# Performance work log

Measured on AMD Instinct MI355X. Metric: run time of the kernel, lower is better.

Reference implementation:

```python
import jax, jax.numpy as jnp
import numpy as np

B, NPG, DEG = 512, 128, 16          # graphs, nodes/graph, out-degree
N = B * NPG                          # 65536 nodes
E = N * DEG                          # 1048576 edges
IN_DIM, HID, HEADS = 11, 32, 4
K1 = int(np.ceil(0.8 * NPG))         # 103 nodes/graph after pool1
K2 = int(np.ceil(0.8 * K1))          # 83 nodes/graph after pool2


def gat_conv(x, src, dst, mask, W, a_s, a_d, b, n_nodes):
    # PyG GATConv (concat=True, add_self_loops=True, eval mode -> no dropout)
    xp = (x @ W).reshape(n_nodes, HEADS, HID)            # [N,H,C]
    as_ = jnp.einsum('nhc,hc->nh', xp, a_s)
    ad_ = jnp.einsum('nhc,hc->nh', xp, a_d)
    loop = jnp.arange(n_nodes)
    s = jnp.concatenate([src, loop])
    d = jnp.concatenate([dst, loop])
    m = jnp.concatenate([mask, jnp.ones(n_nodes, bool)])
    logit = jax.nn.leaky_relu(as_[s] + ad_[d], 0.2)      # [E+N,H]
    logit = jnp.where(m[:, None], logit, -1e9)
    mx = jax.ops.segment_max(logit, d, num_segments=n_nodes)
    ex = jnp.exp(logit - mx[d]) * m[:, None]
    den = jax.ops.segment_sum(ex, d, num_segments=n_nodes)
    alpha = ex / (den[d] + 1e-16)                        # segment softmax over dst
    out = jax.ops.segment_sum(alpha[:, :, None] * xp[s], d, num_segments=n_nodes)
    return out.reshape(n_nodes, HEADS * HID) + b


def topk_pool(x, src, dst, mask, w, npg, k):
    # PyG TopKPooling: score = tanh((x*w).sum(-1)/||w||); keep top ceil(ratio*n) per graph
    nb = x.shape[0] // npg
    score = jnp.tanh((x @ w) / jnp.linalg.norm(w))
    vals, idx = jax.lax.top_k(score.reshape(nb, npg), k)  # [B,k]
    perm = (idx + (jnp.arange(nb) * npg)[:, None]).reshape(-1)
    x_new = x[perm] * vals.reshape(-1, 1)
    remap = jnp.full(nb * npg, -1).at[perm].set(jnp.arange(nb * k))
    ns, nd = remap[src], remap[dst]
    m = mask & (ns >= 0) & (nd >= 0)
    return x_new, jnp.where(m, ns, 0), jnp.where(m, nd, 0), m


def setup_inputs():
    key = jax.random.key(0)
    ks = jax.random.split(key, 24)
    s = 0.05
    x = jax.random.normal(ks[0], (N, IN_DIM), jnp.float32)
    src = jnp.repeat(jnp.arange(N), DEG)
    dst = (src // NPG) * NPG + jax.random.randint(ks[1], (E,), 0, NPG)
    edge_index = jnp.stack([src, dst])
    edge_attr = jax.random.normal(ks[2], (E, 4), jnp.float32)
    batch = jnp.repeat(jnp.arange(B), NPG)
    p = dict(
        W_g1=jax.random.normal(ks[3], (IN_DIM, HEADS * HID), jnp.float32) * s,
        att_src1=jax.random.normal(ks[4], (HEADS, HID), jnp.float32) * s,
        att_dst1=jax.random.normal(ks[5], (HEADS, HID), jnp.float32) * s,
        b_g1=jnp.zeros((HEADS * HID,), jnp.float32),
        W_t1=jax.random.normal(ks[6], (HEADS * HID, HID), jnp.float32) * s,
        b_t1=jnp.zeros((HID,), jnp.float32),
        pool_w1=jax.random.normal(ks[7], (HID,), jnp.float32) * s,
        W_g2=jax.random.normal(ks[8], (HID, HEADS * HID), jnp.float32) * s,
        att_src2=jax.random.normal(ks[9], (HEADS, HID), jnp.float32) * s,
        att_dst2=jax.random.normal(ks[10], (HEADS, HID), jnp.float32) * s,
        b_g2=jnp.zeros((HEADS * HID,), jnp.float32),
        W_t2=jax.random.normal(ks[11], (HEADS * HID, HID), jnp.float32) * s,
        b_t2=jnp.zeros((HID,), jnp.float32),
        pool_w2=jax.random.normal(ks[12], (HID,), jnp.float32) * s,
        W_l1=jax.random.normal(ks[13], (2 * HID, 256), jnp.float32) * s,
        b_l1=jnp.zeros((256,), jnp.float32),
        W_l2=jax.random.normal(ks[14], (256, 1024), jnp.float32) * s,
        b_l2=jnp.zeros((1024,), jnp.float32),
        W_l3=jax.random.normal(ks[15], (1024, 1), jnp.float32) * s,
        b_l3=jnp.zeros((1,), jnp.float32),
    )
    return dict(x=x, edge_index=edge_index, edge_attr=edge_attr, batch=batch, **p)


def reference(x, edge_index, edge_attr, batch,
              W_g1, att_src1, att_dst1, b_g1, W_t1, b_t1, pool_w1,
              W_g2, att_src2, att_dst2, b_g2, W_t2, b_t2, pool_w2,
              W_l1, b_l1, W_l2, b_l2, W_l3, b_l3):
    # edge_attr is ignored (GATConv built without edge_dim); batch is implicit
    # in the fixed equal-size graph layout.  Eval mode -> dropout disabled.
    src, dst = edge_index[0], edge_index[1]
    mask = jnp.ones(E, bool)
    h = jax.nn.relu(gat_conv(x, src, dst, mask, W_g1, att_src1, att_dst1, b_g1, N))
    h = h @ W_t1 + b_t1
    h, src, dst, mask = topk_pool(h, src, dst, mask, pool_w1, NPG, K1)
    h1 = h.reshape(B, K1, HID)
    g1 = jnp.concatenate([h1.max(1), h1.mean(1)], axis=1)   # [B, 2*HID]
    h = jax.nn.relu(gat_conv(h, src, dst, mask, W_g2, att_src2, att_dst2, b_g2, B * K1))
    h = h @ W_t2 + b_t2
    h, src, dst, mask = topk_pool(h, src, dst, mask, pool_w2, K1, K2)
    h2 = h.reshape(B, K2, HID)
    g2 = jnp.concatenate([h2.max(1), h2.mean(1)], axis=1)
    g = g1 + g2
    g = jax.nn.relu(g @ W_l1 + b_l1)
    g = jax.nn.relu(g @ W_l2 + b_l2)
    return g @ W_l3 + b_l3                                   # [B,1]
```

## Files before the change

kernel.cpp:

```cpp
#include <hip/hip_runtime.h>
#include <math.h>

constexpr int NPGc  = 128;
constexpr int NG    = 512;
constexpr int EPGc  = 2048;
constexpr int ETOT  = 1048576;
constexpr int IND   = 11;
constexpr int HIDc  = 32;
constexpr int FD    = 128;
constexpr int K1c   = 103;
constexpr int K2c   = 83;
constexpr int NN    = NG * NPGc;
constexpr int N2c   = NG * K1c;

__device__ __forceinline__ float lrelu(float x){ return fmaxf(x, 0.2f*x); }

__device__ __forceinline__ unsigned flipF(float f){
    unsigned u = __float_as_uint(f);
    return u ^ (unsigned)(((int)u >> 31) | 0x80000000);
}
__device__ __forceinline__ float unflipF(unsigned u){
    unsigned m = ((u >> 31) - 1u) | 0x80000000u;
    return __uint_as_float(u ^ m);
}

template<int KIN>
__device__ void foldDev(const float* __restrict__ Wg, const float* __restrict__ avs,
                        const float* __restrict__ avd, float* __restrict__ S, float* __restrict__ D, int t)
{
    if (t < KIN * 4) {
        int k = t >> 2, h = t & 3;
        float s = 0.f, d = 0.f;
        for (int j = 0; j < HIDc; j++) {
            float w = Wg[k*FD + h*HIDc + j];
            s = fmaf(w, avs[h*HIDc + j], s);
            d = fmaf(w, avd[h*HIDc + j], d);
        }
        S[t] = s; D[t] = d;
    }
}
__global__ void k_fold2(const float* W1, const float* s1, const float* d1, float* S1, float* D1,
                        const float* W2, const float* s2, const float* d2, float* S2, float* D2)
{
    if (blockIdx.x == 0) foldDev<IND>(W1, s1, d1, S1, D1, threadIdx.x);
    else                 foldDev<HIDc>(W2, s2, d2, S2, D2, threadIdx.x);
}

template<bool REMAP>
__global__ __launch_bounds__(256) void k_csr(const int* __restrict__ ei, const int* __restrict__ rankv,
                                             int* __restrict__ csrOff, unsigned char* __restrict__ csrSB,
                                             unsigned char* __restrict__ csrDB, int nnode)
{
    int g = blockIdx.x, t = threadIdx.x;
    __shared__ int cnt[128], cur[128], offL[129];
    __shared__ unsigned char sbL[EPGc], dbL[EPGc];
    __shared__ signed char rmap[NPGc];
    if (t < 128) cnt[t] = 0;
    if constexpr (REMAP) { if (t < NPGc) rmap[t] = (signed char)rankv[g*NPGc + t]; }
    __syncthreads();
    const int* dstG = ei + ETOT + g * EPGc;
    int sn[8], dn[8];
    #pragma unroll
    for (int q = 0; q < 8; q++) {
        int e = t + 256*q;
        int dO = dstG[e] - g * NPGc, s0 = e >> 4;
        if constexpr (REMAP) {
            int s = rmap[s0], d = rmap[dO];
            bool ok = (s >= 0 && d >= 0);
            sn[q] = s; dn[q] = ok ? d : -1;
        } else { sn[q] = s0; dn[q] = dO; }
        if (dn[q] >= 0) atomicAdd(&cnt[dn[q]], 1);
    }
    __syncthreads();
    if (t < 64) {
        int c0 = cnt[2*t], c1 = cnt[2*t + 1], ps = c0 + c1, P = ps;
        #pragma unroll
        for (int dlt = 1; dlt < 64; dlt <<= 1) { int v = __shfl_up(P, dlt); if (t >= dlt) P += v; }
        int E0 = P - ps;
        offL[2*t] = E0; offL[2*t + 1] = E0 + c0;
        cur[2*t] = E0; cur[2*t + 1] = E0 + c0;
        if (t == 63) offL[128] = P;
    }
    __syncthreads();
    #pragma unroll
    for (int q = 0; q < 8; q++) {
        if (dn[q] >= 0) {
            int pos = atomicAdd(&cur[dn[q]], 1);
            sbL[pos] = (unsigned char)sn[q];
            dbL[pos] = (unsigned char)dn[q];
        }
    }
    __syncthreads();
    if (t < 128) {
        ((int4*)(csrSB + (size_t)g * EPGc))[t] = ((const int4*)sbL)[t];
        ((int4*)(csrDB + (size_t)g * EPGc))[t] = ((const int4*)dbL)[t];
    }
    if (t <= nnode) csrOff[g*132 + t] = offL[t];
}

template<int NNODE, int KIN, int KEEP, bool FIRST>
__global__ __launch_bounds__(256, 4) void k_layer(
    const float* __restrict__ xin, const float* __restrict__ Wg,
    const float* __restrict__ WsS, const float* __restrict__ WsD,
    const float* __restrict__ bg,
    const float* __restrict__ Wt, const float* __restrict__ bt,
    const float* __restrict__ pw,
    const int* __restrict__ csrOff, const unsigned char* __restrict__ csrSB,
    const unsigned char* __restrict__ csrDB,
    float* __restrict__ xnew, int* __restrict__ rankv,
    float* __restrict__ gfeat, const float* __restrict__ gprev)
{
    constexpr int NP   = (NNODE + 3) & ~3;
    constexpr int NGRP = NP / 4;
    int g = blockIdx.x, t = threadIdx.x;

    __shared__ __align__(16) float xFT[KIN * NP];
    __shared__ __align__(16) float WfL[KIN * FD];
    __shared__ __align__(16) float WtL[FD * HIDc];
    __shared__ __align__(16) float xpL[NP * 36];
    __shared__ float wEu[EPGc];
    __shared__ unsigned char sbL[EPGc], dbL[EPGc];
    __shared__ int offL[NNODE + 1];
    __shared__ float asL[NNODE], adL[NNODE], sfW[NNODE], sDi[NNODE];
    __shared__ unsigned maxU[NNODE];
    __shared__ __align__(8) float admL[NNODE * 2];
    __shared__ float WsSL[KIN * 4], WsDL[KIN * 4], bgL[FD], btL[HIDc];

    {
        const float* xg = xin + (size_t)g * NNODE * KIN;
        for (int i = t; i < NNODE * KIN; i += 256) {
            int n = i / KIN, k = i - n * KIN;
            xFT[k * NP + n] = xg[i];
        }
        if constexpr (NP > NNODE) {
            for (int i = t; i < KIN * (NP - NNODE); i += 256) {
                int k = i / (NP - NNODE), n = NNODE + (i % (NP - NNODE));
                xFT[k * NP + n] = 0.f;
            }
        }
    }
    for (int i = t; i < KIN * FD / 4; i += 256) ((float4*)WfL)[i] = ((const float4*)Wg)[i];
    for (int i = t; i < FD * HIDc / 4; i += 256) ((float4*)WtL)[i] = ((const float4*)Wt)[i];
    for (int i = t; i < KIN * 4; i += 256) { WsSL[i] = WsS[i]; WsDL[i] = WsD[i]; }
    if (t < FD) bgL[t] = bg[t];
    if (t < HIDc) btL[t] = bt[t];
    if (t <= NNODE) offL[t] = csrOff[g*132 + t];
    for (int i = t; i < EPGc / 16; i += 256) {
        ((int4*)sbL)[i] = ((const int4*)(csrSB + (size_t)g * EPGc))[i];
        ((int4*)dbL)[i] = ((const int4*)(csrDB + (size_t)g * EPGc))[i];
    }
    __syncthreads();
    const int EC = offL[NNODE];

    const int n4 = t >> 3, j4 = t & 7;
    float4 acc0, acc1, acc2, acc3;
    { float4 bi = make_float4(btL[j4*4], btL[j4*4+1], btL[j4*4+2], btL[j4*4+3]);
      acc0 = bi; acc1 = bi; acc2 = bi; acc3 = bi; }

    for (int h = 0; h < 4; h++) {
        __syncthreads();

        for (int id = t; id < NGRP * 32; id += 256) {
            int grp = id >> 5, c = id & 31;
            float4 a = make_float4(0.f, 0.f, 0.f, 0.f);
            #pragma unroll
            for (int k = 0; k < KIN; k++) {
                float4 xv = *(const float4*)&xFT[k * NP + grp * 4];
                float w = WfL[k * FD + h * 32 + c];
                a.x = fmaf(xv.x, w, a.x); a.y = fmaf(xv.y, w, a.y);
                a.z = fmaf(xv.z, w, a.z); a.w = fmaf(xv.w, w, a.w);
            }
            int nb = grp * 4;
            xpL[(nb+0)*36 + c] = a.x; xpL[(nb+1)*36 + c] = a.y;
            xpL[(nb+2)*36 + c] = a.z; xpL[(nb+3)*36 + c] = a.w;
        }
        if (t < NNODE) {
            float s = 0.f, d = 0.f;
            #pragma unroll
            for (int k = 0; k < KIN; k++) {
                float v = xFT[k * NP + t];
                s = fmaf(v, WsSL[k*4 + h], s);
                d = fmaf(v, WsDL[k*4 + h], d);
            }
            asL[t] = s; adL[t] = d; maxU[t] = flipF(s);
        }
        __syncthreads();

        for (int s = t; s < EC; s += 256)
            atomicMax(&maxU[dbL[s]], flipF(asL[sbL[s]]));
        __syncthreads();

        if (t < NNODE) {
            float ad = adL[t];
            float m = lrelu(unflipF(maxU[t]) + ad);
            admL[2*t] = ad; admL[2*t + 1] = m;
            sfW[t] = expf(lrelu(asL[t] + ad) - m);
        }
        __syncthreads();

        for (int s = t; s < EC; s += 256) {
            int sb = sbL[s], db = dbL[s];
            float2 am = *(const float2*)&admL[2*db];
            wEu[s] = expf(lrelu(asL[sb] + am.x) - am.y);
        }
        __syncthreads();

        if (t < NNODE) {
            float den = sfW[t];
            int lo = offL[t], hi = offL[t + 1];
            for (int s = lo; s < hi; s++) den += wEu[s];
            sDi[t] = 1.f / (den + 1e-16f);
        }
        __syncthreads();

        const float4* X4 = (const float4*)xpL;
        auto aggOne = [&](int p) -> float4 {
            int n = p >> 3, c4 = p & 7;
            float w0 = sfW[n];
            float4 v = X4[n*9 + c4];
            float4 a; a.x = w0*v.x; a.y = w0*v.y; a.z = w0*v.z; a.w = w0*v.w;
            int lo = offL[n], hi = offL[n + 1];
            for (int s = lo; s < hi; s++) {
                int sc = sbL[s]; float w = wEu[s];
                float4 u = X4[sc*9 + c4];
                a.x = fmaf(w, u.x, a.x); a.y = fmaf(w, u.y, a.y);
                a.z = fmaf(w, u.z, a.z); a.w = fmaf(w, u.w, a.w);
            }
            float inv = sDi[n];
            float4 r;
            r.x = fmaxf(fmaf(a.x, inv, bgL[h*32 + c4*4 + 0]), 0.f);
            r.y = fmaxf(fmaf(a.y, inv, bgL[h*32 + c4*4 + 1]), 0.f);
            r.z = fmaxf(fmaf(a.z, inv, bgL[h*32 + c4*4 + 2]), 0.f);
            r.w = fmaxf(fmaf(a.w, inv, bgL[h*32 + c4*4 + 3]), 0.f);
            return r;
        };
        float4 rv0 = aggOne(t);
        float4 rv1 = aggOne(t + 256);
        float4 rv2 = aggOne(t + 512);
        float4 rv3;
        if (t + 768 < NNODE * 8) rv3 = aggOne(t + 768);
        __syncthreads();

        float4* X4w = (float4*)xpL;
        X4w[(t>>3)*9 + (t&7)] = rv0;
        { int p = t + 256; X4w[(p>>3)*9 + (p&7)] = rv1; }
        { int p = t + 512; X4w[(p>>3)*9 + (p&7)] = rv2; }
        if (t + 768 < NNODE * 8) { int p = t + 768; X4w[(p>>3)*9 + (p&7)] = rv3; }
        __syncthreads();

        if (n4 < NGRP) {
            int nb = n4 * 4;
            #pragma unroll 8
            for (int c = 0; c < 32; c++) {
                float4 w4 = *(const float4*)&WtL[(h*32 + c)*HIDc + j4*4];
                float r0 = xpL[(nb+0)*36 + c], r1 = xpL[(nb+1)*36 + c];
                float r2 = xpL[(nb+2)*36 + c], r3 = xpL[(nb+3)*36 + c];
                acc0.x = fmaf(r0, w4.x, acc0.x); acc0.y = fmaf(r0, w4.y, acc0.y);
                acc0.z = fmaf(r0, w4.z, acc0.z); acc0.w = fmaf(r0, w4.w, acc0.w);
                acc1.x = fmaf(r1, w4.x, acc1.x); acc1.y = fmaf(r1, w4.y, acc1.y);
                acc1.z = fmaf(r1, w4.z, acc1.z); acc1.w = fmaf(r1, w4.w, acc1.w);
                acc2.x = fmaf(r2, w4.x, acc2.x); acc2.y = fmaf(r2, w4.y, acc2.y);
                acc2.z = fmaf(r2, w4.z, acc2.z); acc2.w = fmaf(r2, w4.w, acc2.w);
                acc3.x = fmaf(r3, w4.x, acc3.x); acc3.y = fmaf(r3, w4.y, acc3.y);
                acc3.z = fmaf(r3, w4.z, acc3.z); acc3.w = fmaf(r3, w4.w, acc3.w);
            }
        }
    }
    __syncthreads();

    float* htL = xpL;
    if (n4 < NGRP) {
        int nb = n4 * 4, jb = j4 * 4;
        float4 av[4] = {acc0, acc1, acc2, acc3};
        #pragma unroll
        for (int i = 0; i < 4; i++) {
            int n = nb + i;
            if (n < NNODE) {
                htL[n*33 + jb + 0] = av[i].x; htL[n*33 + jb + 1] = av[i].y;
                htL[n*33 + jb + 2] = av[i].z; htL[n*33 + jb + 3] = av[i].w;
            }
        }
    }
    __syncthreads();

    float* scoreL = wEu;
    int*   rnkL   = (int*)(wEu + 128);
    float nrm; { float ss = 0.f; for (int k = 0; k < HIDc; k++) { float w = pw[k]; ss = fmaf(w, w, ss); } nrm = sqrtf(ss); }
    if (t < NNODE) {
        float dot = 0.f;
        for (int k = 0; k < HIDc; k++) dot = fmaf(htL[t*33 + k], pw[k], dot);
        scoreL[t] = tanhf(dot / nrm);
    }
    __syncthreads();
    if (t < NNODE) {
        float si = scoreL[t]; int rank = 0;
        for (int q = 0; q < NNODE; q++) {
            float sj = scoreL[q];
            rank += (sj > si || (sj == si && q < t)) ? 1 : 0;
        }
        rnkL[t] = (rank < KEEP) ? rank : -1;
        if (FIRST) rankv[g*NPGc + t] = rnkL[t];
    }
    __syncthreads();
    if (FIRST) {
        for (int p = t; p < NNODE * 32; p += 256) {
            int n = p >> 5, jj = p & 31;
            int rk = rnkL[n];
            if (rk >= 0) xnew[((size_t)g*KEEP + rk)*HIDc + jj] = htL[n*33 + jj] * scoreL[n];
        }
    }
    if (t < HIDc) {
        float mx = -INFINITY, sm = 0.f;
        for (int n = 0; n < NNODE; n++) {
            if (rnkL[n] >= 0) { float v = htL[n*33 + t] * scoreL[n]; mx = fmaxf(mx, v); sm += v; }
        }
        float mean = sm / (float)KEEP;
        if (FIRST) {
            gfeat[(size_t)g*64 + t]      = mx;
            gfeat[(size_t)g*64 + 32 + t] = mean;
        } else {
            gfeat[(size_t)g*64 + t]      = gprev[(size_t)g*64 + t] + mx;
            gfeat[(size_t)g*64 + 32 + t] = gprev[(size_t)g*64 + 32 + t] + mean;
        }
    }
}

__global__ __launch_bounds__(256) void k_mlpA(const float* __restrict__ gsum,
    const float* __restrict__ W1, const float* __restrict__ b1,
    const float* __restrict__ W2, const float* __restrict__ b2,
    const float* __restrict__ W3, float* __restrict__ part)
{
    int gb = blockIdx.x, q = blockIdx.y, t = threadIdx.x;
    int g0 = gb * 4;
    __shared__ float gL[256];
    __shared__ float h1L[1024];
    __shared__ float4 red[256];
    gL[t] = gsum[(size_t)g0*64 + t];
    __syncthreads();
    float bv = b1[t];
    float a0 = bv, a1 = bv, a2 = bv, a3 = bv;
    #pragma unroll 4
    for (int k = 0; k < 64; k++) {
        float w = W1[k*256 + t];
        a0 = fmaf(gL[k], w, a0); a1 = fmaf(gL[64 + k], w, a1);
        a2 = fmaf(gL[128 + k], w, a2); a3 = fmaf(gL[192 + k], w, a3);
    }
    h1L[t] = fmaxf(a0, 0.f); h1L[256 + t] = fmaxf(a1, 0.f);
    h1L[512 + t] = fmaxf(a2, 0.f); h1L[768 + t] = fmaxf(a3, 0.f);
    __syncthreads();
    int o = q * 256 + t;
    float b2v = b2[o], w3 = W3[o];
    float c0 = b2v, c1 = b2v, c2 = b2v, c3 = b2v;
    const float* w2c = W2 + o;
    #pragma unroll 8
    for (int i = 0; i < 256; i++) {
        float w = w2c[(size_t)i * 1024];
        c0 = fmaf(h1L[i], w, c0); c1 = fmaf(h1L[256 + i], w, c1);
        c2 = fmaf(h1L[512 + i], w, c2); c3 = fmaf(h1L[768 + i], w, c3);
    }
    red[t] = make_float4(fmaxf(c0, 0.f)*w3, fmaxf(c1, 0.f)*w3, fmaxf(c2, 0.f)*w3, fmaxf(c3, 0.f)*w3);
    __syncthreads();
    for (int s = 128; s > 0; s >>= 1) {
        if (t < s) { float4 a = red[t], b = red[t + s]; a.x += b.x; a.y += b.y; a.z += b.z; a.w += b.w; red[t] = a; }
        __syncthreads();
    }
    if (t == 0) {
        float4 r = red[0];
        part[(size_t)(g0 + 0)*4 + q] = r.x;
        part[(size_t)(g0 + 1)*4 + q] = r.y;
        part[(size_t)(g0 + 2)*4 + q] = r.z;
        part[(size_t)(g0 + 3)*4 + q] = r.w;
    }
}

__global__ void k_mlpB(const float* __restrict__ part, const float* __restrict__ b3,
                       float* __restrict__ outp)
{
    int g = blockIdx.x * 256 + threadIdx.x;
    if (g < NG) {
        float4 p = ((const float4*)part)[g];
        outp[g] = ((p.x + p.y) + (p.z + p.w)) + b3[0];
    }
}

extern "C" void kernel_launch(void* const* d_in, const int* in_sizes, int n_in,
                              void* d_out, int out_size, void* d_ws, size_t ws_size,
                              hipStream_t stream)
{
    const float* x    = (const float*)d_in[0];
    const int*   ei   = (const int*)  d_in[1];
    const float* W_g1 = (const float*)d_in[4];
    const float* as1w = (const float*)d_in[5];
    const float* ad1w = (const float*)d_in[6];
    const float* b_g1 = (const float*)d_in[7];
    const float* W_t1 = (const float*)d_in[8];
    const float* b_t1 = (const float*)d_in[9];
    const float* pw1  = (const float*)d_in[10];
    const float* W_g2 = (const float*)d_in[11];
    const float* as2w = (const float*)d_in[12];
    const float* ad2w = (const float*)d_in[13];
    const float* b_g2 = (const float*)d_in[14];
    const float* W_t2 = (const float*)d_in[15];
    const float* b_t2 = (const float*)d_in[16];
    const float* pw2  = (const float*)d_in[17];
    const float* W_l1 = (const float*)d_in[18];
    const float* b_l1 = (const float*)d_in[19];
    const float* W_l2 = (const float*)d_in[20];
    const float* b_l2 = (const float*)d_in[21];
    const float* W_l3 = (const float*)d_in[22];
    const float* b_l3 = (const float*)d_in[23];
    float* out = (float*)d_out;

    char* ws = (char*)d_ws;
    size_t off = 0;
    auto alloc = [&](size_t bytes) -> void* {
        void* p = (void*)(ws + off);
        off += ((bytes + 255) / 256) * 256;
        return p;
    };
    float* x2    = (float*)alloc((size_t)N2c * HIDc * 4);
    int*   rank1 = (int*)  alloc((size_t)NN * 4);
    float* g1    = (float*)alloc((size_t)NG * 64 * 4);
    float* gsum  = (float*)alloc((size_t)NG * 64 * 4);
    float* part  = (float*)alloc((size_t)NG * 4 * 4);
    float* wsS1  = (float*)alloc(64 * 4);
    float* wsD1  = (float*)alloc(64 * 4);
    float* wsS2  = (float*)alloc(128 * 4);
    float* wsD2  = (float*)alloc(128 * 4);
    int*   off1  = (int*)  alloc((size_t)NG * 132 * 4);
    unsigned char* sb1 = (unsigned char*)alloc((size_t)NG * EPGc);
    unsigned char* db1 = (unsigned char*)alloc((size_t)NG * EPGc);
    int*   off2  = (int*)  alloc((size_t)NG * 132 * 4);
    unsigned char* sb2 = (unsigned char*)alloc((size_t)NG * EPGc);
    unsigned char* db2 = (unsigned char*)alloc((size_t)NG * EPGc);

    k_fold2<<<2, 128, 0, stream>>>(W_g1, as1w, ad1w, wsS1, wsD1,
                                   W_g2, as2w, ad2w, wsS2, wsD2);
    k_csr<false><<<NG, 256, 0, stream>>>(ei, nullptr, off1, sb1, db1, NPGc);

    k_layer<NPGc, IND, K1c, true><<<NG, 256, 0, stream>>>(
        x, W_g1, wsS1, wsD1, b_g1, W_t1, b_t1, pw1,
        off1, sb1, db1, x2, rank1, g1, nullptr);

    k_csr<true><<<NG, 256, 0, stream>>>(ei, rank1, off2, sb2, db2, K1c);

    k_layer<K1c, HIDc, K2c, false><<<NG, 256, 0, stream>>>(
        x2, W_g2, wsS2, wsD2, b_g2, W_t2, b_t2, pw2,
        off2, sb2, db2, nullptr, nullptr, gsum, g1);

    k_mlpA<<<dim3(NG/4, 4), 256, 0, stream>>>(gsum, W_l1, b_l1, W_l2, b_l2, W_l3, part);
    k_mlpB<<<2, 256, 0, stream>>>(part, b_l3, out);
}
```

Baseline: 315.2 us.

## Fuse CSR build, attention fold and MLP head into the two layer kernels

Cuts the pipeline from seven launches to two. The first layer now builds its CSR in shared memory and writes the remapped CSR for layer two directly from its own top-k ranks. The second layer runs the MLP head per graph in its epilogue, and attention logits now come from the projected features instead of precomputed folded weights. Per-head weight slices are staged into smaller shared buffers to reduce LDS use, but the fused MLP recomputes the large W2 product one graph per block with poor reuse of W2 loads, which can be slower than the batched 4-graph MLP kernel.

```diff
diff --git a/kernel.cpp b/kernel.cpp
--- a/kernel.cpp
+++ b/kernel.cpp
@@ -24,107 +24,41 @@
     return __uint_as_float(u ^ m);
 }
 
-template<int KIN>
-__device__ void foldDev(const float* __restrict__ Wg, const float* __restrict__ avs,
-                        const float* __restrict__ avd, float* __restrict__ S, float* __restrict__ D, int t)
-{
-    if (t < KIN * 4) {
-        int k = t >> 2, h = t & 3;
-        float s = 0.f, d = 0.f;
-        for (int j = 0; j < HIDc; j++) {
-            float w = Wg[k*FD + h*HIDc + j];
-            s = fmaf(w, avs[h*HIDc + j], s);
-            d = fmaf(w, avd[h*HIDc + j], d);
-        }
-        S[t] = s; D[t] = d;
-    }
-}
-__global__ void k_fold2(const float* W1, const float* s1, const float* d1, float* S1, float* D1,
-                        const float* W2, const float* s2, const float* d2, float* S2, float* D2)
-{
-    if (blockIdx.x == 0) foldDev<IND>(W1, s1, d1, S1, D1, threadIdx.x);
-    else                 foldDev<HIDc>(W2, s2, d2, S2, D2, threadIdx.x);
-}
-
-template<bool REMAP>
-__global__ __launch_bounds__(256) void k_csr(const int* __restrict__ ei, const int* __restrict__ rankv,
-                                             int* __restrict__ csrOff, unsigned char* __restrict__ csrSB,
-                                             unsigned char* __restrict__ csrDB, int nnode)
-{
-    int g = blockIdx.x, t = threadIdx.x;
-    __shared__ int cnt[128], cur[128], offL[129];
-    __shared__ unsigned char sbL[EPGc], dbL[EPGc];
-    __shared__ signed char rmap[NPGc];
-    if (t < 128) cnt[t] = 0;
-    if constexpr (REMAP) { if (t < NPGc) rmap[t] = (signed char)rankv[g*NPGc + t]; }
-    __syncthreads();
-    const int* dstG = ei + ETOT + g * EPGc;
-    int sn[8], dn[8];
-    #pragma unroll
-    for (int q = 0; q < 8; q++) {
-        int e = t + 256*q;
-        int dO = dstG[e] - g * NPGc, s0 = e >> 4;
-        if constexpr (REMAP) {
-            int s = rmap[s0], d = rmap[dO];
-            bool ok = (s >= 0 && d >= 0);
-            sn[q] = s; dn[q] = ok ? d : -1;
-        } else { sn[q] = s0; dn[q] = dO; }
-        if (dn[q] >= 0) atomicAdd(&cnt[dn[q]], 1);
-    }
-    __syncthreads();
-    if (t < 64) {
-        int c0 = cnt[2*t], c1 = cnt[2*t + 1], ps = c0 + c1, P = ps;
-        #pragma unroll
-        for (int dlt = 1; dlt < 64; dlt <<= 1) { int v = __shfl_up(P, dlt); if (t >= dlt) P += v; }
-        int E0 = P - ps;
-        offL[2*t] = E0; offL[2*t + 1] = E0 + c0;
-        cur[2*t] = E0; cur[2*t + 1] = E0 + c0;
-        if (t == 63) offL[128] = P;
-    }
-    __syncthreads();
-    #pragma unroll
-    for (int q = 0; q < 8; q++) {
-        if (dn[q] >= 0) {
-            int pos = atomicAdd(&cur[dn[q]], 1);
-            sbL[pos] = (unsigned char)sn[q];
-            dbL[pos] = (unsigned char)dn[q];
-        }
-    }
-    __syncthreads();
-    if (t < 128) {
-        ((int4*)(csrSB + (size_t)g * EPGc))[t] = ((const int4*)sbL)[t];
-        ((int4*)(csrDB + (size_t)g * EPGc))[t] = ((const int4*)dbL)[t];
-    }
-    if (t <= nnode) csrOff[g*132 + t] = offL[t];
-}
-
 template<int NNODE, int KIN, int KEEP, bool FIRST>
 __global__ __launch_bounds__(256, 4) void k_layer(
     const float* __restrict__ xin, const float* __restrict__ Wg,
-    const float* __restrict__ WsS, const float* __restrict__ WsD,
+    const float* __restrict__ avs, const float* __restrict__ avd,
     const float* __restrict__ bg,
     const float* __restrict__ Wt, const float* __restrict__ bt,
     const float* __restrict__ pw,
-    const int* __restrict__ csrOff, const unsigned char* __restrict__ csrSB,
-    const unsigned char* __restrict__ csrDB,
-    float* __restrict__ xnew, int* __restrict__ rankv,
-    float* __restrict__ gfeat, const float* __restrict__ gprev)
+    const int* __restrict__ ei,
+    int* __restrict__ csrOffW, unsigned char* __restrict__ sbW,
+    unsigned char* __restrict__ dbW,
+    const int* __restrict__ csrOffR, const unsigned char* __restrict__ sbR,
+    const unsigned char* __restrict__ dbR,
+    float* __restrict__ xnew,
+    float* __restrict__ gfeat, const float* __restrict__ gprev,
+    const float* __restrict__ W1, const float* __restrict__ b1,
+    const float* __restrict__ W2, const float* __restrict__ b2,
+    const float* __restrict__ W3, const float* __restrict__ b3,
+    float* __restrict__ outp)
 {
     constexpr int NP   = (NNODE + 3) & ~3;
     constexpr int NGRP = NP / 4;
     int g = blockIdx.x, t = threadIdx.x;
 
     __shared__ __align__(16) float xFT[KIN * NP];
-    __shared__ __align__(16) float WfL[KIN * FD];
-    __shared__ __align__(16) float WtL[FD * HIDc];
     __shared__ __align__(16) float xpL[NP * 36];
-    __shared__ float wEu[EPGc];
-    __shared__ unsigned char sbL[EPGc], dbL[EPGc];
-    __shared__ int offL[NNODE + 1];
+    __shared__ __align__(16) float wEu[EPGc];
+    __shared__ __align__(16) unsigned char sbL[EPGc], dbL[EPGc];
+    __shared__ int offL[129];
     __shared__ float asL[NNODE], adL[NNODE], sfW[NNODE], sDi[NNODE];
     __shared__ unsigned maxU[NNODE];
-    __shared__ __align__(8) float admL[NNODE * 2];
-    __shared__ float WsSL[KIN * 4], WsDL[KIN * 4], bgL[FD], btL[HIDc];
+    __shared__ __align__(16) float WgsL[KIN * 32];
+    __shared__ __align__(16) float WtsL[1024];
+    __shared__ float avsL[FD], avdL[FD], bgL[FD], btL[HIDc];
+    __shared__ float gvec[64];
+    float* mLn = (float*)maxU;
 
     {
         const float* xg = xin + (size_t)g * NNODE * KIN;
@@ -139,25 +73,58 @@
             }
         }
     }
-    for (int i = t; i < KIN * FD / 4; i += 256) ((float4*)WfL)[i] = ((const float4*)Wg)[i];
-    for (int i = t; i < FD * HIDc / 4; i += 256) ((float4*)WtL)[i] = ((const float4*)Wt)[i];
-    for (int i = t; i < KIN * 4; i += 256) { WsSL[i] = WsS[i]; WsDL[i] = WsD[i]; }
-    if (t < FD) bgL[t] = bg[t];
+    if (t < FD)   { avsL[t] = avs[t]; avdL[t] = avd[t]; bgL[t] = bg[t]; }
     if (t < HIDc) btL[t] = bt[t];
-    if (t <= NNODE) offL[t] = csrOff[g*132 + t];
-    for (int i = t; i < EPGc / 16; i += 256) {
-        ((int4*)sbL)[i] = ((const int4*)(csrSB + (size_t)g * EPGc))[i];
-        ((int4*)dbL)[i] = ((const int4*)(csrDB + (size_t)g * EPGc))[i];
+
+    if constexpr (FIRST) {
+        int* cnt = (int*)maxU;
+        int* cur = (int*)sfW;
+        if (t < 128) cnt[t] = 0;
+        __syncthreads();
+        const int* dstG = ei + ETOT + g * EPGc;
+        int dnv[8];
+        #pragma unroll
+        for (int q = 0; q < 8; q++) {
+            int e = t + 256*q;
+            dnv[q] = dstG[e] - g * NPGc;
+            atomicAdd(&cnt[dnv[q]], 1);
+        }
+        __syncthreads();
+        if (t < 64) {
+            int c0 = cnt[2*t], c1 = cnt[2*t + 1], ps = c0 + c1, P = ps;
+            #pragma unroll
+            for (int dl = 1; dl < 64; dl <<= 1) { int v = __shfl_up(P, dl); if (t >= dl) P += v; }
+            int E0 = P - ps;
+            offL[2*t] = E0; offL[2*t + 1] = E0 + c0;
+            cur[2*t]  = E0; cur[2*t + 1]  = E0 + c0;
+            if (t == 63) offL[128] = P;
+        }
+        __syncthreads();
+        #pragma unroll
+        for (int q = 0; q < 8; q++) {
+            int e = t + 256*q;
+            int pos = atomicAdd(&cur[dnv[q]], 1);
+            sbL[pos] = (unsigned char)(e >> 4);
+            dbL[pos] = (unsigned char)dnv[q];
+        }
+    } else {
+        if (t <= NNODE) offL[t] = csrOffR[g*132 + t];
+        for (int i = t; i < EPGc / 16; i += 256) {
+            ((int4*)sbL)[i] = ((const int4*)(sbR + (size_t)g * EPGc))[i];
+            ((int4*)dbL)[i] = ((const int4*)(dbR + (size_t)g * EPGc))[i];
+        }
     }
     __syncthreads();
     const int EC = offL[NNODE];
 
-    const int n4 = t >> 3, j4 = t & 7;
+    const int n0 = t >> 3, j4 = t & 7;
     float4 acc0, acc1, acc2, acc3;
     { float4 bi = make_float4(btL[j4*4], btL[j4*4+1], btL[j4*4+2], btL[j4*4+3]);
       acc0 = bi; acc1 = bi; acc2 = bi; acc3 = bi; }
 
     for (int h = 0; h < 4; h++) {
+        for (int i = t; i < KIN * 32; i += 256) WgsL[i] = Wg[(i >> 5)*FD + h*32 + (i & 31)];
+        ((float4*)WtsL)[t] = ((const float4*)(Wt + h*1024))[t];
         __syncthreads();
 
         for (int id = t; id < NGRP * 32; id += 256) {
@@ -166,7 +133,7 @@
             #pragma unroll
             for (int k = 0; k < KIN; k++) {
                 float4 xv = *(const float4*)&xFT[k * NP + grp * 4];
-                float w = WfL[k * FD + h * 32 + c];
+                float w = WgsL[k*32 + c];
                 a.x = fmaf(xv.x, w, a.x); a.y = fmaf(xv.y, w, a.y);
                 a.z = fmaf(xv.z, w, a.z); a.w = fmaf(xv.w, w, a.w);
             }
@@ -174,15 +141,19 @@
             xpL[(nb+0)*36 + c] = a.x; xpL[(nb+1)*36 + c] = a.y;
             xpL[(nb+2)*36 + c] = a.z; xpL[(nb+3)*36 + c] = a.w;
         }
-        if (t < NNODE) {
-            float s = 0.f, d = 0.f;
-            #pragma unroll
-            for (int k = 0; k < KIN; k++) {
-                float v = xFT[k * NP + t];
-                s = fmaf(v, WsSL[k*4 + h], s);
-                d = fmaf(v, WsDL[k*4 + h], d);
-            }
-            asL[t] = s; adL[t] = d; maxU[t] = flipF(s);
+        __syncthreads();
+
+        for (int p = t; p < NNODE * 8; p += 256) {
+            int n = p >> 3, jo = p & 7;
+            float4 v = ((const float4*)xpL)[n*9 + jo];
+            const float* As = &avsL[h*32 + jo*4];
+            const float* Ad = &avdL[h*32 + jo*4];
+            float s = v.x*As[0]; s = fmaf(v.y, As[1], s); s = fmaf(v.z, As[2], s); s = fmaf(v.w, As[3], s);
+            float d = v.x*Ad[0]; d = fmaf(v.y, Ad[1], d); d = fmaf(v.z, Ad[2], d); d = fmaf(v.w, Ad[3], d);
+            s += __shfl_xor(s, 1); d += __shfl_xor(d, 1);
+            s += __shfl_xor(s, 2); d += __shfl_xor(d, 2);
+            s += __shfl_xor(s, 4); d += __shfl_xor(d, 4);
+            if (jo == 0) { asL[n] = s; adL[n] = d; maxU[n] = flipF(s); }
         }
         __syncthreads();
 
@@ -193,15 +164,14 @@
         if (t < NNODE) {
             float ad = adL[t];
             float m = lrelu(unflipF(maxU[t]) + ad);
-            admL[2*t] = ad; admL[2*t + 1] = m;
             sfW[t] = expf(lrelu(asL[t] + ad) - m);
+            mLn[t] = m;
         }
         __syncthreads();
 
         for (int s = t; s < EC; s += 256) {
             int sb = sbL[s], db = dbL[s];
-            float2 am = *(const float2*)&admL[2*db];
-            wEu[s] = expf(lrelu(asL[sb] + am.x) - am.y);
+            wEu[s] = expf(lrelu(asL[sb] + adL[db]) - mLn[db]);
         }
         __syncthreads();
 
@@ -214,72 +184,91 @@
         __syncthreads();
 
         const float4* X4 = (const float4*)xpL;
-        auto aggOne = [&](int p) -> float4 {
-            int n = p >> 3, c4 = p & 7;
-            float w0 = sfW[n];
-            float4 v = X4[n*9 + c4];
-            float4 a; a.x = w0*v.x; a.y = w0*v.y; a.z = w0*v.z; a.w = w0*v.w;
-            int lo = offL[n], hi = offL[n + 1];
-            for (int s = lo; s < hi; s++) {
-                int sc = sbL[s]; float w = wEu[s];
-                float4 u = X4[sc*9 + c4];
-                a.x = fmaf(w, u.x, a.x); a.y = fmaf(w, u.y, a.y);
-                a.z = fmaf(w, u.z, a.z); a.w = fmaf(w, u.w, a.w);
-            }
-            float inv = sDi[n];
-            float4 r;
-            r.x = fmaxf(fmaf(a.x, inv, bgL[h*32 + c4*4 + 0]), 0.f);
-            r.y = fmaxf(fmaf(a.y, inv, bgL[h*32 + c4*4 + 1]), 0.f);
-            r.z = fmaxf(fmaf(a.z, inv, bgL[h*32 + c4*4 + 2]), 0.f);
-            r.w = fmaxf(fmaf(a.w, inv, bgL[h*32 + c4*4 + 3]), 0.f);
-            return r;
-        };
-        float4 rv0 = aggOne(t);
-        float4 rv1 = aggOne(t + 256);
-        float4 rv2 = aggOne(t + 512);
-        float4 rv3;
-        if (t + 768 < NNODE * 8) rv3 = aggOne(t + 768);
-        __syncthreads();
-
-        float4* X4w = (float4*)xpL;
-        X4w[(t>>3)*9 + (t&7)] = rv0;
-        { int p = t + 256; X4w[(p>>3)*9 + (p&7)] = rv1; }
-        { int p = t + 512; X4w[(p>>3)*9 + (p&7)] = rv2; }
-        if (t + 768 < NNODE * 8) { int p = t + 768; X4w[(p>>3)*9 + (p&7)] = rv3; }
-        __syncthreads();
-
-        if (n4 < NGRP) {
-            int nb = n4 * 4;
-            #pragma unroll 8
-            for (int c = 0; c < 32; c++) {
-                float4 w4 = *(const float4*)&WtL[(h*32 + c)*HIDc + j4*4];
-                float r0 = xpL[(nb+0)*36 + c], r1 = xpL[(nb+1)*36 + c];
-                float r2 = xpL[(nb+2)*36 + c], r3 = xpL[(nb+3)*36 + c];
-                acc0.x = fmaf(r0, w4.x, acc0.x); acc0.y = fmaf(r0, w4.y, acc0.y);
-                acc0.z = fmaf(r0, w4.z, acc0.z); acc0.w = fmaf(r0, w4.w, acc0.w);
-                acc1.x = fmaf(r1, w4.x, acc1.x); acc1.y = fmaf(r1, w4.y, acc1.y);
-                acc1.z = fmaf(r1, w4.z, acc1.z); acc1.w = fmaf(r1, w4.w, acc1.w);
-                acc2.x = fmaf(r2, w4.x, acc2.x); acc2.y = fmaf(r2, w4.y, acc2.y);
-                acc2.z = fmaf(r2, w4.z, acc2.z); acc2.w = fmaf(r2, w4.w, acc2.w);
-                acc3.x = fmaf(r3, w4.x, acc3.x); acc3.y = fmaf(r3, w4.y, acc3.y);
-                acc3.z = fmaf(r3, w4.z, acc3.z); acc3.w = fmaf(r3, w4.w, acc3.w);
-            }
-        }
-    }
-    __syncthreads();
+        float4 rv[4];
+        #pragma unroll
+        for (int r = 0; r < 4; r++) {
+            int p = t + r*256;
+            if (p < NNODE * 8) {
+                int n = p >> 3, c4 = p & 7;
+                float w0 = sfW[n];
+                float4 v = X4[n*9 + c4];
+                float4 a; a.x = w0*v.x; a.y = w0*v.y; a.z = w0*v.z; a.w = w0*v.w;
+                int lo = offL[n], hi = offL[n + 1];
+                for (int s = lo; s < hi; s++) {
+                    int sc = sbL[s]; float w = wEu[s];
+                    float4 u = X4[sc*9 + c4];
+                    a.x = fmaf(w, u.x, a.x); a.y = fmaf(w, u.y, a.y);
+                    a.z = fmaf(w, u.z, a.z); a.w = fmaf(w, u.w, a.w);
+                }
+                float inv = sDi[n];
+                rv[r].x = fmaxf(fmaf(a.x, inv, bgL[h*32 + c4*4 + 0]), 0.f);
+                rv[r].y = fmaxf(fmaf(a.y, inv, bgL[h*32 + c4*4 + 1]), 0.f);
+                rv[r].z = fmaxf(fmaf(a.z, inv, bgL[h*32 + c4*4 + 2]), 0.f);
+                rv[r].w = fmaxf(fmaf(a.w, inv, bgL[h*32 + c4*4 + 3]), 0.f);
+            }
+        }
+        __syncthreads();
+        {
+            float4* X4w = (float4*)xpL;
+            #pragma unroll
+            for (int r = 0; r < 4; r++) {
+                int p = t + r*256;
+                if (p < NNODE * 8) X4w[(p>>3)*9 + (p&7)] = rv[r];
+            }
+        }
+        __syncthreads();
+
+        #pragma unroll
+        for (int c4 = 0; c4 < 8; c4++) {
+            float4 w0 = *(const float4*)&WtsL[(c4*4 + 0)*32 + j4*4];
+            float4 w1 = *(const float4*)&WtsL[(c4*4 + 1)*32 + j4*4];
+            float4 w2 = *(const float4*)&WtsL[(c4*4 + 2)*32 + j4*4];
+            float4 w3 = *(const float4*)&WtsL[(c4*4 + 3)*32 + j4*4];
+            {
+                float4 xv = X4[n0*9 + c4];
+                acc0.x = fmaf(xv.x,w0.x, fmaf(xv.y,w1.x, fmaf(xv.z,w2.x, fmaf(xv.w,w3.x, acc0.x))));
+                acc0.y = fmaf(xv.x,w0.y, fmaf(xv.y,w1.y, fmaf(xv.z,w2.y, fmaf(xv.w,w3.y, acc0.y))));
+                acc0.z = fmaf(xv.x,w0.z, fmaf(xv.y,w1.z, fmaf(xv.z,w2.z, fmaf(xv.w,w3.z, acc0.z))));
+                acc0.w = fmaf(xv.x,w0.w, fmaf(xv.y,w1.w, fmaf(xv.z,w2.w, fmaf(xv.w,w3.w, acc0.w))));
+            }
+            if (n0 + 32 < NNODE) {
+                float4 xv = X4[(n0+32)*9 + c4];
+                acc1.x = fmaf(xv.x,w0.x, fmaf(xv.y,w1.x, fmaf(xv.z,w2.x, fmaf(xv.w,w3.x, acc1.x))));
+                acc1.y = fmaf(xv.x,w0.y, fmaf(xv.y,w1.y, fmaf(xv.z,w2.y, fmaf(xv.w,w3.y, acc1.y))));
+                acc1.z = fmaf(xv.x,w0.z, fmaf(xv.y,w1.z, fmaf(xv.z,w2.z, fmaf(xv.w,w3.z, acc1.z))));
+                acc1.w = fmaf(xv.x,w0.w, fmaf(xv.y,w1.w, fmaf(xv.z,w2.w, fmaf(xv.w,w3.w, acc1.w))));
+            }
+            if (n0 + 64 < NNODE) {
+                float4 xv = X4[(n0+64)*9 + c4];
+                acc2.x = fmaf(xv.x,w0.x, fmaf(xv.y,w1.x, fmaf(xv.z,w2.x, fmaf(xv.w,w3.x, acc2.x))));
+                acc2.y = fmaf(xv.x,w0.y, fmaf(xv.y,w1.y, fmaf(xv.z,w2.y, fmaf(xv.w,w3.y, acc2.y))));
+                acc2.z = fmaf(xv.x,w0.z, fmaf(xv.y,w1.z, fmaf(xv.z,w2.z, fmaf(xv.w,w3.z, acc2.z))));
+                acc2.w = fmaf(xv.x,w0.w, fmaf(xv.y,w1.w, fmaf(xv.z,w2.w, fmaf(xv.w,w3.w, acc2.w))));
+            }
+            if (n0 + 96 < NNODE) {
+                float4 xv = X4[(n0+96)*9 + c4];
+                acc3.x = fmaf(xv.x,w0.x, fmaf(xv.y,w1.x, fmaf(xv.z,w2.x, fmaf(xv.w,w3.x, acc3.x))));
+                acc3.y = fmaf(xv.x,w0.y, fmaf(xv.y,w1.y, fmaf(xv.z,w2.y, fmaf(xv.w,w3.y, acc3.y))));
+                acc3.z = fmaf(xv.x,w0.z, fmaf(xv.y,w1.z, fmaf(xv.z,w2.z, fmaf(xv.w,w3.z, acc3.z))));
+                acc3.w = fmaf(xv.x,w0.w, fmaf(xv.y,w1.w, fmaf(xv.z,w2.w, fmaf(xv.w,w3.w, acc3.w))));
+            }
+        }
+        __syncthreads();
+    }
 
     float* htL = xpL;
-    if (n4 < NGRP) {
-        int nb = n4 * 4, jb = j4 * 4;
-        float4 av[4] = {acc0, acc1, acc2, acc3};
-        #pragma unroll
-        for (int i = 0; i < 4; i++) {
-            int n = nb + i;
-            if (n < NNODE) {
-                htL[n*33 + jb + 0] = av[i].x; htL[n*33 + jb + 1] = av[i].y;
-                htL[n*33 + jb + 2] = av[i].z; htL[n*33 + jb + 3] = av[i].w;
-            }
-        }
+    {
+        htL[n0*33 + j4*4 + 0] = acc0.x; htL[n0*33 + j4*4 + 1] = acc0.y;
+        htL[n0*33 + j4*4 + 2] = acc0.z; htL[n0*33 + j4*4 + 3] = acc0.w;
+        int n = n0 + 32;
+        if (n < NNODE) { htL[n*33 + j4*4 + 0] = acc1.x; htL[n*33 + j4*4 + 1] = acc1.y;
+                         htL[n*33 + j4*4 + 2] = acc1.z; htL[n*33 + j4*4 + 3] = acc1.w; }
+        n = n0 + 64;
+        if (n < NNODE) { htL[n*33 + j4*4 + 0] = acc2.x; htL[n*33 + j4*4 + 1] = acc2.y;
+                         htL[n*33 + j4*4 + 2] = acc2.z; htL[n*33 + j4*4 + 3] = acc2.w; }
+        n = n0 + 96;
+        if (n < NNODE) { htL[n*33 + j4*4 + 0] = acc3.x; htL[n*33 + j4*4 + 1] = acc3.y;
+                         htL[n*33 + j4*4 + 2] = acc3.z; htL[n*33 + j4*4 + 3] = acc3.w; }
     }
     __syncthreads();
 
@@ -299,10 +288,9 @@
             rank += (sj > si || (sj == si && q < t)) ? 1 : 0;
         }
         rnkL[t] = (rank < KEEP) ? rank : -1;
-        if (FIRST) rankv[g*NPGc + t] = rnkL[t];
     }
     __syncthreads();
-    if (FIRST) {
+    if constexpr (FIRST) {
         for (int p = t; p < NNODE * 32; p += 256) {
             int n = p >> 5, jj = p & 31;
             int rk = rnkL[n];
@@ -315,71 +303,78 @@
             if (rnkL[n] >= 0) { float v = htL[n*33 + t] * scoreL[n]; mx = fmaxf(mx, v); sm += v; }
         }
         float mean = sm / (float)KEEP;
-        if (FIRST) {
+        if constexpr (FIRST) {
             gfeat[(size_t)g*64 + t]      = mx;
             gfeat[(size_t)g*64 + 32 + t] = mean;
         } else {
-            gfeat[(size_t)g*64 + t]      = gprev[(size_t)g*64 + t] + mx;
-            gfeat[(size_t)g*64 + 32 + t] = gprev[(size_t)g*64 + 32 + t] + mean;
-        }
-    }
-}
-
-__global__ __launch_bounds__(256) void k_mlpA(const float* __restrict__ gsum,
-    const float* __restrict__ W1, const float* __restrict__ b1,
-    const float* __restrict__ W2, const float* __restrict__ b2,
-    const float* __restrict__ W3, float* __restrict__ part)
-{
-    int gb = blockIdx.x, q = blockIdx.y, t = threadIdx.x;
-    int g0 = gb * 4;
-    __shared__ float gL[256];
-    __shared__ float h1L[1024];
-    __shared__ float4 red[256];
-    gL[t] = gsum[(size_t)g0*64 + t];
-    __syncthreads();
-    float bv = b1[t];
-    float a0 = bv, a1 = bv, a2 = bv, a3 = bv;
-    #pragma unroll 4
-    for (int k = 0; k < 64; k++) {
-        float w = W1[k*256 + t];
-        a0 = fmaf(gL[k], w, a0); a1 = fmaf(gL[64 + k], w, a1);
-        a2 = fmaf(gL[128 + k], w, a2); a3 = fmaf(gL[192 + k], w, a3);
-    }
-    h1L[t] = fmaxf(a0, 0.f); h1L[256 + t] = fmaxf(a1, 0.f);
-    h1L[512 + t] = fmaxf(a2, 0.f); h1L[768 + t] = fmaxf(a3, 0.f);
-    __syncthreads();
-    int o = q * 256 + t;
-    float b2v = b2[o], w3 = W3[o];
-    float c0 = b2v, c1 = b2v, c2 = b2v, c3 = b2v;
-    const float* w2c = W2 + o;
-    #pragma unroll 8
-    for (int i = 0; i < 256; i++) {
-        float w = w2c[(size_t)i * 1024];
-        c0 = fmaf(h1L[i], w, c0); c1 = fmaf(h1L[256 + i], w, c1);
-        c2 = fmaf(h1L[512 + i], w, c2); c3 = fmaf(h1L[768 + i], w, c3);
-    }
-    red[t] = make_float4(fmaxf(c0, 0.f)*w3, fmaxf(c1, 0.f)*w3, fmaxf(c2, 0.f)*w3, fmaxf(c3, 0.f)*w3);
-    __syncthreads();
-    for (int s = 128; s > 0; s >>= 1) {
-        if (t < s) { float4 a = red[t], b = red[t + s]; a.x += b.x; a.y += b.y; a.z += b.z; a.w += b.w; red[t] = a; }
-        __syncthreads();
-    }
-    if (t == 0) {
-        float4 r = red[0];
-        part[(size_t)(g0 + 0)*4 + q] = r.x;
-        part[(size_t)(g0 + 1)*4 + q] = r.y;
-        part[(size_t)(g0 + 2)*4 + q] = r.z;
-        part[(size_t)(g0 + 3)*4 + q] = r.w;
-    }
-}
-
-__global__ void k_mlpB(const float* __restrict__ part, const float* __restrict__ b3,
-                       float* __restrict__ outp)
-{
-    int g = blockIdx.x * 256 + threadIdx.x;
-    if (g < NG) {
-        float4 p = ((const float4*)part)[g];
-        outp[g] = ((p.x + p.y) + (p.z + p.w)) + b3[0];
+            gvec[t]      = gprev[(size_t)g*64 + t] + mx;
+            gvec[32 + t] = gprev[(size_t)g*64 + 32 + t] + mean;
+        }
+    }
+
+    if constexpr (FIRST) {
+        __syncthreads();
+        int* cnt = (int*)maxU;
+        int* cur = (int*)sfW;
+        if (t < 128) cnt[t] = 0;
+        __syncthreads();
+        const int* dstG = ei + ETOT + g * EPGc;
+        int snv[8], dnv[8];
+        #pragma unroll
+        for (int q = 0; q < 8; q++) {
+            int e = t + 256*q;
+            int s = rnkL[e >> 4], d = rnkL[dstG[e] - g * NPGc];
+            bool ok = (s >= 0 && d >= 0);
+            snv[q] = s; dnv[q] = ok ? d : -1;
+            if (ok) atomicAdd(&cnt[d], 1);
+        }
+        __syncthreads();
+        if (t < 64) {
+            int c0 = cnt[2*t], c1 = cnt[2*t + 1], ps = c0 + c1, P = ps;
+            #pragma unroll
+            for (int dl = 1; dl < 64; dl <<= 1) { int v = __shfl_up(P, dl); if (t >= dl) P += v; }
+            int E0 = P - ps;
+            offL[2*t] = E0; offL[2*t + 1] = E0 + c0;
+            cur[2*t]  = E0; cur[2*t + 1]  = E0 + c0;
+            if (t == 63) offL[128] = P;
+        }
+        __syncthreads();
+        #pragma unroll
+        for (int q = 0; q < 8; q++) {
+            if (dnv[q] >= 0) {
+                int pos = atomicAdd(&cur[dnv[q]], 1);
+                sbL[pos] = (unsigned char)snv[q];
+                dbL[pos] = (unsigned char)dnv[q];
+            }
+        }
+        __syncthreads();
+        if (t < 128) {
+            ((int4*)(sbW + (size_t)g * EPGc))[t] = ((const int4*)sbL)[t];
+            ((int4*)(dbW + (size_t)g * EPGc))[t] = ((const int4*)dbL)[t];
+        }
+        if (t <= K1c) csrOffW[g*132 + t] = offL[t];
+    } else {
+        __syncthreads();
+        float* h1L = wEu;
+        float* red = wEu + 256;
+        float a = b1[t];
+        #pragma unroll 4
+        for (int k = 0; k < 64; k++) a = fmaf(gvec[k], W1[k*256 + t], a);
+        h1L[t] = fmaxf(a, 0.f);
+        __syncthreads();
+        float p = 0.f;
+        for (int q = 0; q < 4; q++) {
+            int o = t + q*256;
+            float c = b2[o];
+            const float* w2c = W2 + o;
+            #pragma unroll 4
+            for (int i = 0; i < 256; i++) c = fmaf(h1L[i], w2c[(size_t)i * 1024], c);
+            p = fmaf(fmaxf(c, 0.f), W3[o], p);
+        }
+        red[t] = p;
+        __syncthreads();
+        for (int s = 128; s > 0; s >>= 1) { if (t < s) red[t] += red[t + s]; __syncthreads(); }
+        if (t == 0) outp[g] = red[0] + b3[0];
     }
 }
 
@@ -418,36 +413,21 @@
         off += ((bytes + 255) / 256) * 256;
         return p;
     };
-    float* x2    = (float*)alloc((size_t)N2c * HIDc * 4);
-    int*   rank1 = (int*)  alloc((size_t)NN * 4);
-    float* g1    = (float*)alloc((size_t)NG * 64 * 4);
-    float* gsum  = (float*)alloc((size_t)NG * 64 * 4);
-    float* part  = (float*)alloc((size_t)NG * 4 * 4);
-    float* wsS1  = (float*)alloc(64 * 4);
-    float* wsD1  = (float*)alloc(64 * 4);
-    float* wsS2  = (float*)alloc(128 * 4);
-    float* wsD2  = (float*)alloc(128 * 4);
-    int*   off1  = (int*)  alloc((size_t)NG * 132 * 4);
-    unsigned char* sb1 = (unsigned char*)alloc((size_t)NG * EPGc);
-    unsigned char* db1 = (unsigned char*)alloc((size_t)NG * EPGc);
-    int*   off2  = (int*)  alloc((size_t)NG * 132 * 4);
+    float* x2   = (float*)alloc((size_t)N2c * HIDc * 4);
+    float* g1   = (float*)alloc((size_t)NG * 64 * 4);
+    int*   off2 = (int*)  alloc((size_t)NG * 132 * 4);
     unsigned char* sb2 = (unsigned char*)alloc((size_t)NG * EPGc);
     unsigned char* db2 = (unsigned char*)alloc((size_t)NG * EPGc);
 
-    k_fold2<<<2, 128, 0, stream>>>(W_g1, as1w, ad1w, wsS1, wsD1,
-                                   W_g2, as2w, ad2w, wsS2, wsD2);
-    k_csr<false><<<NG, 256, 0, stream>>>(ei, nullptr, off1, sb1, db1, NPGc);
-
     k_layer<NPGc, IND, K1c, true><<<NG, 256, 0, stream>>>(
-        x, W_g1, wsS1, wsD1, b_g1, W_t1, b_t1, pw1,
-        off1, sb1, db1, x2, rank1, g1, nullptr);
-
-    k_csr<true><<<NG, 256, 0, stream>>>(ei, rank1, off2, sb2, db2, K1c);
+        x, W_g1, as1w, ad1w, b_g1, W_t1, b_t1, pw1,
+        ei, off2, sb2, db2, nullptr, nullptr, nullptr,
+        x2, g1, nullptr,
+        nullptr, nullptr, nullptr, nullptr, nullptr, nullptr, nullptr);
 
     k_layer<K1c, HIDc, K2c, false><<<NG, 256, 0, stream>>>(
-        x2, W_g2, wsS2, wsD2, b_g2, W_t2, b_t2, pw2,
-        off2, sb2, db2, nullptr, nullptr, gsum, g1);
-
-    k_mlpA<<<dim3(NG/4, 4), 256, 0, stream>>>(gsum, W_l1, b_l1, W_l2, b_l2, W_l3, part);
-    k_mlpB<<<2, 256, 0, stream>>>(part, b_l3, out);
+        x2, W_g2, as2w, ad2w, b_g2, W_t2, b_t2, pw2,
+        nullptr, nullptr, nullptr, nullptr, off2, sb2, db2,
+        nullptr, nullptr, g1,
+        W_l1, b_l1, W_l2, b_l2, W_l3, b_l3, out);
 }
```

New measurement: 443.2 us. +40.6%, slower.
